# Optimization experiments

Hardware: AMD Instinct MI355X
Metric: run time of the kernel (lower is better)

Reference implementation:

```python
import jax, jax.numpy as jnp
import numpy as np

B, C_IN, HW = 4096, 3, 32
NUM_MODULES, NUM_AGENTS, OUT_DIM = 16, 10, 10
FEAT = 128
HID = 48
BN_EPS = 1e-5


def _conv_block(x, w, b):
    # x: [B,C,H,W], w: [O,I,3,3] -> conv(pad=1) + ReLU + maxpool2
    y = jax.lax.conv_general_dilated(
        x, w, window_strides=(1, 1), padding=((1, 1), (1, 1)),
        dimension_numbers=("NCHW", "OIHW", "NCHW"))
    y = jax.nn.relu(y + b[None, :, None, None])
    return jax.lax.reduce_window(y, -jnp.inf, jax.lax.max,
                                 (1, 1, 2, 2), (1, 1, 2, 2), "VALID")


def setup_inputs() -> dict:
    key = jax.random.key(0)
    ks = jax.random.split(key, 24)

    def lin(k, shape, fan_in):
        return (jax.random.normal(k, shape, dtype=jnp.float32) / np.sqrt(fan_in)).astype(jnp.float32)

    inp = {
        "x": jax.random.normal(ks[0], (B, C_IN, HW, HW), dtype=jnp.float32),
        "tasks": jax.random.randint(ks[1], (B,), 0, NUM_AGENTS, dtype=jnp.int32),
        # conv backbone
        "cw1": lin(ks[2], (32, C_IN, 3, 3), C_IN * 9), "cb1": jnp.zeros((32,), jnp.float32),
        "cw2": lin(ks[3], (32, 32, 3, 3), 32 * 9),     "cb2": jnp.zeros((32,), jnp.float32),
        "cw3": lin(ks[4], (32, 32, 3, 3), 32 * 9),     "cb3": jnp.zeros((32,), jnp.float32),
        "cw4": lin(ks[5], (32, 32, 3, 3), 32 * 9),     "cb4": jnp.zeros((32,), jnp.float32),
        "bn_g": jnp.ones((32,), jnp.float32), "bn_b": jnp.zeros((32,), jnp.float32),
        # routing policies (approx linear policies)
        "wpt": lin(ks[6], (FEAT, NUM_AGENTS), FEAT),                  # per-task assignment (1 agent)
        "wd1": lin(ks[7], (NUM_AGENTS, FEAT, NUM_MODULES), FEAT),    # per-agent decision 1
        "wd2": lin(ks[8], (NUM_AGENTS, HID, NUM_MODULES), HID),      # per-agent decision 2
        "wd3": lin(ks[9], (NUM_AGENTS, HID, NUM_MODULES), HID),      # per-agent decision 3
        # expert banks (stacked Linear layers, stored [in,out])
        "s1_w": lin(ks[10], (NUM_MODULES, FEAT, HID), FEAT), "s1_b": jnp.zeros((NUM_MODULES, HID), jnp.float32),
        "s2_w": lin(ks[11], (NUM_MODULES, HID, HID), HID),   "s2_b": jnp.zeros((NUM_MODULES, HID), jnp.float32),
        "s3_w": lin(ks[12], (NUM_MODULES, HID, OUT_DIM), HID), "s3_b": jnp.zeros((NUM_MODULES, OUT_DIM), jnp.float32),
    }
    return inp


def _decide(feat, wd, agents):
    # gather per-sample agent policy, pick argmax action
    logits = jnp.einsum("bf,bfm->bm", feat, wd[agents])  # [B, num_modules]
    return jnp.argmax(logits, axis=-1)


def _select(feat, w_bank, b_bank, actions, relu=True):
    # per-sample expert gather -> small GEMM -> scatter back (vectorized)
    y = jnp.einsum("bf,bfo->bo", feat, w_bank[actions]) + b_bank[actions]
    return jax.nn.relu(y) if relu else y


def reference(x, tasks, cw1, cb1, cw2, cb2, cw3, cb3, cw4, cb4, bn_g, bn_b,
              wpt, wd1, wd2, wd3, s1_w, s1_b, s2_w, s2_b, s3_w, s3_b):
    y = _conv_block(x, cw1, cb1)
    y = _conv_block(y, cw2, cb2)
    y = _conv_block(y, cw3, cb3)
    y = _conv_block(y, cw4, cb4)
    # BatchNorm2d (training-mode batch stats)
    mu = jnp.mean(y, axis=(0, 2, 3), keepdims=True)
    var = jnp.var(y, axis=(0, 2, 3), keepdims=True)
    y = (y - mu) * jax.lax.rsqrt(var + BN_EPS) * bn_g[None, :, None, None] + bn_b[None, :, None, None]
    y = y.reshape(y.shape[0], -1)  # [B, 128]

    # per-task assignment: single-agent policy picks the agent id per sample
    task_actions = jnp.argmax(y @ wpt, axis=-1)  # [B]

    a1 = _decide(y, wd1, task_actions)
    y = _select(y, s1_w, s1_b, a1, relu=True)
    a2 = _decide(y, wd2, task_actions)
    y = _select(y, s2_w, s2_b, a2, relu=True)
    a3 = _decide(y, wd3, task_actions)
    y = _select(y, s3_w, s3_b, a3, relu=False)
    return y
```

## Files before the change

kernel.cpp:

```cpp
#include <hip/hip_runtime.h>
#include <math.h>


#define IMG_B 4096

typedef _Float16 f16x8 __attribute__((ext_vector_type(8)));
typedef _Float16 f16x4 __attribute__((ext_vector_type(4)));
typedef float    f32x4 __attribute__((ext_vector_type(4)));

union U16x8 { unsigned u[4]; f16x8 v; };

__device__ inline f16x8 f16x8_zero() {
    f16x8 z;
    #pragma unroll
    for (int i = 0; i < 8; ++i) z[i] = (_Float16)0.f;
    return z;
}

__global__ __launch_bounds__(256) void twt_kernel(
    const float* __restrict__ cw1, const float* __restrict__ cw2,
    const float* __restrict__ cw3, const float* __restrict__ cw4,
    _Float16* __restrict__ w1s, _Float16* __restrict__ w2s,
    _Float16* __restrict__ w3s, _Float16* __restrict__ w4s)
{
    const int i = blockIdx.x * 256 + threadIdx.x;
    if (i < 2048) {
        const int p = i >> 10, rr = i & 1023;
        const int oc = rr >> 5, k = rr & 31;
        _Float16 val = (_Float16)0.f;
        if (k < 27) {
            float w = cw1[oc * 27 + k];
            _Float16 h = (_Float16)w;
            val = p ? (_Float16)(w - (float)h) : h;
        }
        w1s[p * 1024 + oc * 32 + k] = val;
    }
    if (i < 9216) {
        const int k = i % 9, r = i / 9;
        const int ic2 = r & 31, oc2 = r >> 5;
        {
            float w = cw2[(oc2 * 32 + ic2) * 9 + k];
            _Float16 h = (_Float16)w;
            w2s[(k * 2 + 0) * 1024 + oc2 * 32 + ic2] = h;
            w2s[(k * 2 + 1) * 1024 + oc2 * 32 + ic2] = (_Float16)(w - (float)h);
        }
        {
            float w = cw3[(oc2 * 32 + ic2) * 9 + k];
            _Float16 h = (_Float16)w;
            w3s[(k * 2 + 0) * 1024 + oc2 * 32 + ic2] = h;
            w3s[(k * 2 + 1) * 1024 + oc2 * 32 + ic2] = (_Float16)(w - (float)h);
        }
        {
            float w = cw4[(oc2 * 32 + ic2) * 9 + k];
            _Float16 h = (_Float16)w;
            w4s[(k * 2 + 0) * 1024 + oc2 * 32 + ic2] = h;
            w4s[(k * 2 + 1) * 1024 + oc2 * 32 + ic2] = (_Float16)(w - (float)h);
        }
    }
}

__global__ __launch_bounds__(512, 6) void backbone_kernel(
    const float* __restrict__ x,
    const _Float16* __restrict__ w1s, const float* __restrict__ cb1,
    const _Float16* __restrict__ w2s, const float* __restrict__ cb2,
    const _Float16* __restrict__ w3s, const float* __restrict__ cb3,
    const _Float16* __restrict__ w4s, const float* __restrict__ cb4,
    float* __restrict__ t4)
{
    __shared__ __align__(16) unsigned char smem[50736];
    _Float16* b1h = (_Float16*)smem;
    _Float16* b1l = (_Float16*)(smem + 18432);
    unsigned char* region2 = smem + 36864;
    unsigned* sxu = (unsigned*)region2;
    _Float16* b2h = (_Float16*)region2;
    _Float16* b2l = (_Float16*)(region2 + 4096);
    _Float16* b3h = (_Float16*)(region2 + 8192);
    _Float16* b3l = (_Float16*)(region2 + 10496);
    float*    scr = (float*)region2;

    const int t = threadIdx.x;
    const int b = blockIdx.x;
    const int lane = t & 63;
    const int w  = __builtin_amdgcn_readfirstlane(t >> 6);
    const int wr = w >> 1;
    const int mh = w & 1;
    const int xl = lane & 15;
    const int g  = lane >> 4;
    const int aoff = xl * 32 + g * 8;

    for (int i = t; i < 396; i += 512) {
        const int p = i / 132, r = i - p * 132;
        int row, col;
        if (r < 34)       { row = 0;       col = r; }
        else if (r < 68)  { row = 33;      col = r - 34; }
        else if (r < 100) { row = r - 67;  col = 0; }
        else              { row = r - 99;  col = 33; }
        sxu[p * 1156 + row * 34 + col] = 0;
    }
    for (int i = t; i < 1024; i += 512) {
        const int j = i & 15, cs = (i >> 4) & 1, r = (i >> 5) & 15, P = i >> 9;
        ((unsigned*)(smem + P * 18432))[(r * 18 + (cs ? 17 : 0)) * 16 + j] = 0;
    }
    {
        const float* xb = x + (size_t)b * 3072;
        for (int i = t; i < 3072; i += 512) {
            const int ic = i >> 10, r = i & 1023;
            const float v = xb[i];
            const _Float16 h = (_Float16)v;
            const _Float16 l = (_Float16)(v - (float)h);
            const unsigned hu = (unsigned)__builtin_bit_cast(unsigned short, h);
            const unsigned lu = (unsigned)__builtin_bit_cast(unsigned short, l);
            sxu[ic * 1156 + ((r >> 5) + 1) * 34 + (r & 31) + 1] =
                __builtin_amdgcn_perm(lu, hu, 0x05040100u);
        }
    }
    __syncthreads();

    {
        const f16x8 ah0 = *(const f16x8*)(w1s + xl * 32 + g * 8);
        const f16x8 ah1 = *(const f16x8*)(w1s + (16 + xl) * 32 + g * 8);
        const f16x8 al0 = *(const f16x8*)(w1s + 1024 + xl * 32 + g * 8);
        const f16x8 al1 = *(const f16x8*)(w1s + 1024 + (16 + xl) * 32 + g * 8);
        const f32x4 cbias0 = *(const f32x4*)(cb1 + g * 4);
        const f32x4 cbias1 = *(const f32x4*)(cb1 + 16 + g * 4);

        int off_j[8];
        #pragma unroll
        for (int j = 0; j < 8; ++j) {
            int k = g * 8 + j; if (k > 26) k = 26;
            const int ic = k / 9, t9 = k - ic * 9;
            const int dy = t9 / 3, dx = t9 - dy * 3;
            off_j[j] = ic * 1156 + dy * 34 + dx;
        }

        for (int q = 0; q < 2; ++q) {
            const int rp = w * 2 + q;
            const int y0 = 2 * rp;
            for (int xt = 0; xt < 2; ++xt) {
                const int xpix = xt * 16 + xl;
                f32x4 acc[2][2];
                #pragma unroll
                for (int yy = 0; yy < 2; ++yy)
                    #pragma unroll
                    for (int m = 0; m < 2; ++m)
                        #pragma unroll
                        for (int r = 0; r < 4; ++r) acc[yy][m][r] = 0.f;
                #pragma unroll
                for (int yy = 0; yy < 2; ++yy) {
                    const int base = (y0 + yy) * 34 + xpix;
                    unsigned e[8];
                    #pragma unroll
                    for (int j = 0; j < 8; ++j) e[j] = sxu[off_j[j] + base];
                    U16x8 Bh, Bl;
                    #pragma unroll
                    for (int p = 0; p < 4; ++p) {
                        const unsigned e0 = e[2 * p], e1 = e[2 * p + 1];
                        Bh.u[p] = __builtin_amdgcn_perm(e1, e0, 0x05040100u);
                        Bl.u[p] = __builtin_amdgcn_perm(e1, e0, 0x07060302u);
                    }
                    acc[yy][0] = __builtin_amdgcn_mfma_f32_16x16x32_f16(ah0, Bh.v, acc[yy][0], 0, 0, 0);
                    acc[yy][0] = __builtin_amdgcn_mfma_f32_16x16x32_f16(ah0, Bl.v, acc[yy][0], 0, 0, 0);
                    acc[yy][0] = __builtin_amdgcn_mfma_f32_16x16x32_f16(al0, Bh.v, acc[yy][0], 0, 0, 0);
                    acc[yy][1] = __builtin_amdgcn_mfma_f32_16x16x32_f16(ah1, Bh.v, acc[yy][1], 0, 0, 0);
                    acc[yy][1] = __builtin_amdgcn_mfma_f32_16x16x32_f16(ah1, Bl.v, acc[yy][1], 0, 0, 0);
                    acc[yy][1] = __builtin_amdgcn_mfma_f32_16x16x32_f16(al1, Bh.v, acc[yy][1], 0, 0, 0);
                }
                #pragma unroll
                for (int m = 0; m < 2; ++m) {
                    f32x4 vv;
                    #pragma unroll
                    for (int r = 0; r < 4; ++r) {
                        float v = fmaxf(acc[0][m][r], acc[1][m][r]);
                        v = fmaxf(v, __shfl_xor(v, 1));
                        vv[r] = fmaxf(v + (m ? cbias1[r] : cbias0[r]), 0.f);
                    }
                    if ((xl & 1) == 0) {
                        const int c = xt * 8 + (xl >> 1) + 1;
                        const int grp = m * 2 + (g >> 1);
                        const int so = (grp + (c >> 1)) & 3;
                        const int e = (rp * 18 + c) * 32 + so * 8 + (g & 1) * 4;
                        f16x4 h4, l4;
                        #pragma unroll
                        for (int r = 0; r < 4; ++r) {
                            const _Float16 h = (_Float16)vv[r];
                            h4[r] = h;
                            l4[r] = (_Float16)(vv[r] - (float)h);
                        }
                        *(f16x4*)(b1h + e) = h4;
                        *(f16x4*)(b1l + e) = l4;
                    }
                }
            }
        }
    }
    __syncthreads();

    {
        for (int i = t; i < 1152; i += 512) ((unsigned*)(region2 + 8192))[i] = 0;

        f32x4 acc[2][2];
        #pragma unroll
        for (int j = 0; j < 2; ++j)
            #pragma unroll
            for (int m = 0; m < 2; ++m)
                #pragma unroll
                for (int r = 0; r < 4; ++r) acc[j][m][r] = 0.f;

        #pragma unroll
        for (int dy = 0; dy < 3; ++dy) {
            #pragma unroll
            for (int dx = 0; dx < 3; ++dx) {
                const _Float16* wb = w2s + (dy * 3 + dx) * 2048;
                const f16x8 ah0 = *(const f16x8*)(wb + aoff);
                const f16x8 ah1 = *(const f16x8*)(wb + 512 + aoff);
                const f16x8 al0 = *(const f16x8*)(wb + 1024 + aoff);
                const f16x8 al1 = *(const f16x8*)(wb + 1536 + aoff);

                const int cxs = xl + dx;
                const int so = (g + (cxs >> 1)) & 3;
                #pragma unroll
                for (int j = 0; j < 2; ++j) {
                    const int sy = 2 * w + j + dy - 1;
                    if ((unsigned)sy < 16u) {
                        const int e = (sy * 18 + cxs) * 32 + so * 8;
                        const f16x8 bh = *(const f16x8*)(b1h + e);
                        const f16x8 bl = *(const f16x8*)(b1l + e);
                        acc[j][0] = __builtin_amdgcn_mfma_f32_16x16x32_f16(ah0, bh, acc[j][0], 0, 0, 0);
                        acc[j][0] = __builtin_amdgcn_mfma_f32_16x16x32_f16(ah0, bl, acc[j][0], 0, 0, 0);
                        acc[j][0] = __builtin_amdgcn_mfma_f32_16x16x32_f16(al0, bh, acc[j][0], 0, 0, 0);
                        acc[j][1] = __builtin_amdgcn_mfma_f32_16x16x32_f16(ah1, bh, acc[j][1], 0, 0, 0);
                        acc[j][1] = __builtin_amdgcn_mfma_f32_16x16x32_f16(ah1, bl, acc[j][1], 0, 0, 0);
                        acc[j][1] = __builtin_amdgcn_mfma_f32_16x16x32_f16(al1, bh, acc[j][1], 0, 0, 0);
                    }
                }
            }
        }

        const f32x4 bias0 = *(const f32x4*)(cb2 + g * 4);
        const f32x4 bias1 = *(const f32x4*)(cb2 + 16 + g * 4);
        #pragma unroll
        for (int m = 0; m < 2; ++m) {
            f32x4 vv;
            #pragma unroll
            for (int r = 0; r < 4; ++r) {
                float v = fmaxf(acc[0][m][r], acc[1][m][r]);
                v = fmaxf(v, __shfl_xor(v, 1));
                vv[r] = fmaxf(v + (m ? bias1[r] : bias0[r]), 0.f);
            }
            if ((lane & 1) == 0) {
                const int pp = w * 8 + (xl >> 1);
                const int slot = m * 2 + (g >> 1);
                const int so2 = (slot + (pp >> 1)) & 3;
                const int e = pp * 32 + so2 * 8 + (g & 1) * 4;
                f16x4 h4, l4;
                #pragma unroll
                for (int r = 0; r < 4; ++r) {
                    const _Float16 h = (_Float16)vv[r];
                    h4[r] = h;
                    l4[r] = (_Float16)(vv[r] - (float)h);
                }
                *(f16x4*)(b2h + e) = h4;
                *(f16x4*)(b2l + e) = l4;
            }
        }
    }
    __syncthreads();

    {
        const int p = wr * 16 + xl;
        const int py3 = p >> 3, px3 = p & 7;
        f32x4 acc;
        #pragma unroll
        for (int r = 0; r < 4; ++r) acc[r] = 0.f;

        #pragma unroll
        for (int dy = 0; dy < 3; ++dy) {
            #pragma unroll
            for (int dx = 0; dx < 3; ++dx) {
                const _Float16* wb = w3s + (dy * 3 + dx) * 2048 + mh * 512;
                const f16x8 ah = *(const f16x8*)(wb + aoff);
                const f16x8 al = *(const f16x8*)(wb + 1024 + aoff);

                const int syL = py3 + dy - 1, sxL = px3 + dx - 1;
                const bool ok = ((unsigned)syL < 8u) && ((unsigned)sxL < 8u);
                const int cy = syL < 0 ? 0 : (syL > 7 ? 7 : syL);
                const int cx = sxL < 0 ? 0 : (sxL > 7 ? 7 : sxL);
                const int cp = cy * 8 + cx;
                const int so = (g + (cp >> 1)) & 3;
                const int e = cp * 32 + so * 8;
                f16x8 bh = *(const f16x8*)(b2h + e);
                f16x8 bl = *(const f16x8*)(b2l + e);
                if (!ok) { bh = f16x8_zero(); bl = f16x8_zero(); }
                acc = __builtin_amdgcn_mfma_f32_16x16x32_f16(ah, bh, acc, 0, 0, 0);
                acc = __builtin_amdgcn_mfma_f32_16x16x32_f16(ah, bl, acc, 0, 0, 0);
                acc = __builtin_amdgcn_mfma_f32_16x16x32_f16(al, bh, acc, 0, 0, 0);
            }
        }

        const f32x4 bias = *(const f32x4*)(cb3 + mh * 16 + g * 4);
        f32x4 vv;
        #pragma unroll
        for (int r = 0; r < 4; ++r) {
            float v = acc[r];
            v = fmaxf(v, __shfl_xor(v, 1));
            v = fmaxf(v, __shfl_xor(v, 8));
            vv[r] = fmaxf(v + bias[r], 0.f);
        }
        if ((lane & 9) == 0) {
            const int yr = wr;
            const int xr = (xl & 7) >> 1;
            const int pp3 = (yr + 1) * 6 + (xr + 1);
            const int grp = mh * 2 + (g >> 1);
            const int so = (grp + (pp3 >> 1)) & 3;
            const int e = pp3 * 32 + so * 8 + (g & 1) * 4;
            f16x4 h4, l4;
            #pragma unroll
            for (int r = 0; r < 4; ++r) {
                const _Float16 h = (_Float16)vv[r];
                h4[r] = h;
                l4[r] = (_Float16)(vv[r] - (float)h);
            }
            *(f16x4*)(b3h + e) = h4;
            *(f16x4*)(b3l + e) = l4;
        }
    }
    __syncthreads();

    {
        f32x4 a4;
        #pragma unroll
        for (int r = 0; r < 4; ++r) a4[r] = 0.f;

        for (int t9 = wr; t9 < 9; t9 += 4) {
            const _Float16* wb = w4s + t9 * 2048 + mh * 512;
            const f16x8 ah = *(const f16x8*)(wb + aoff);
            const f16x8 al = *(const f16x8*)(wb + 1024 + aoff);
            const int dy = t9 / 3, dx = t9 - dy * 3;
            const int pp3 = ((xl >> 2) + dy) * 6 + (xl & 3) + dx;
            const int so = (g + (pp3 >> 1)) & 3;
            const int e = pp3 * 32 + so * 8;
            const f16x8 bh = *(const f16x8*)(b3h + e);
            const f16x8 bl = *(const f16x8*)(b3l + e);
            a4 = __builtin_amdgcn_mfma_f32_16x16x32_f16(ah, bh, a4, 0, 0, 0);
            a4 = __builtin_amdgcn_mfma_f32_16x16x32_f16(ah, bl, a4, 0, 0, 0);
            a4 = __builtin_amdgcn_mfma_f32_16x16x32_f16(al, bh, a4, 0, 0, 0);
        }
        *(f32x4*)(scr + (w * 64 + lane) * 4) = a4;
        __syncthreads();

        if (w < 2) {
            f32x4 r0;
            #pragma unroll
            for (int r = 0; r < 4; ++r) r0[r] = 0.f;
            #pragma unroll
            for (int k = 0; k < 4; ++k) {
                const f32x4 p0 = *(const f32x4*)(scr + ((k * 2 + w) * 64 + lane) * 4);
                #pragma unroll
                for (int r = 0; r < 4; ++r) r0[r] += p0[r];
            }
            const f32x4 bias = *(const f32x4*)(cb4 + w * 16 + g * 4);
            const int y = xl >> 2, xx = xl & 3;
            f32x4 vv;
            #pragma unroll
            for (int r = 0; r < 4; ++r) {
                float v = r0[r];
                v = fmaxf(v, __shfl_xor(v, 1));
                v = fmaxf(v, __shfl_xor(v, 4));
                vv[r] = fmaxf(v + bias[r], 0.f);
            }
            if ((xl & 5) == 0) {
                const int oc0 = w * 16 + g * 4;
                #pragma unroll
                for (int r = 0; r < 4; ++r)
                    t4[(size_t)b * 128 + (oc0 + r) * 4 + (y >> 1) * 2 + (xx >> 1)] = vv[r];
            }
        }
    }
}

__global__ __launch_bounds__(256) void bnstats_kernel(
    const float* __restrict__ t4, float* __restrict__ mus, float* __restrict__ rss)
{
    __shared__ double ssum[256];
    __shared__ double ssq[256];
    const int c = blockIdx.x, t = threadIdx.x;
    double s = 0.0, q = 0.0;
    for (int j = t; j < 16384; j += 256) {
        float v = t4[(size_t)(j >> 2) * 128 + c * 4 + (j & 3)];
        s += (double)v;
        q += (double)v * (double)v;
    }
    ssum[t] = s; ssq[t] = q;
    __syncthreads();
    for (int w = 128; w > 0; w >>= 1) {
        if (t < w) { ssum[t] += ssum[t + w]; ssq[t] += ssq[t + w]; }
        __syncthreads();
    }
    if (t == 0) {
        double mu = ssum[0] / 16384.0;
        double var = ssq[0] / 16384.0 - mu * mu;
        mus[c] = (float)mu;
        rss[c] = (float)(1.0 / sqrt(var + 1e-5));
    }
}

__device__ __forceinline__ int wave_argmax16(double v, int idx) {
    #pragma unroll
    for (int d = 8; d >= 1; d >>= 1) {
        const double ov = __shfl_xor(v, d);
        const int oi = __shfl_xor(idx, d);
        if (ov > v || (ov == v && oi < idx)) { v = ov; idx = oi; }
    }
    return __shfl(idx, 0);
}

__global__ __launch_bounds__(256) void routing_kernel(
    const float* __restrict__ t4, const float* __restrict__ mus,
    const float* __restrict__ rss,
    const float* __restrict__ bng, const float* __restrict__ bnb,
    const float* __restrict__ wpt, const float* __restrict__ wd1,
    const float* __restrict__ wd2, const float* __restrict__ wd3,
    const float* __restrict__ s1w, const float* __restrict__ s1b,
    const float* __restrict__ s2w, const float* __restrict__ s2b,
    const float* __restrict__ s3w, const float* __restrict__ s3b,
    float* __restrict__ out)
{
    __shared__ float fs[4][128];
    __shared__ float h1s[4][48];
    __shared__ float h2s[4][48];
    const int t = threadIdx.x & 63;
    const int w = threadIdx.x >> 6;
    const int b = blockIdx.x * 4 + w;
    float* fw  = fs[w];
    float* h1w = h1s[w];
    float* h2w = h2s[w];

    for (int i = t; i < 128; i += 64) {
        const int c = i >> 2;
        const float v = t4[(size_t)b * 128 + i];
        fw[i] = (v - mus[c]) * rss[c] * bng[c] + bnb[c];
    }
    __builtin_amdgcn_wave_barrier();

    double a = -INFINITY;
    if (t < 10) {
        a = 0.0;
        for (int k = 0; k < 128; ++k) a = fma((double)fw[k], (double)wpt[k * 10 + t], a);
    }
    const int agent = wave_argmax16(a, t & 15);

    a = -INFINITY;
    if (t < 16) {
        a = 0.0;
        const float* wd = wd1 + (size_t)agent * 2048 + t;
        for (int k = 0; k < 128; ++k) a = fma((double)fw[k], (double)wd[k * 16], a);
    }
    const int a1 = wave_argmax16(a, t & 15);

    if (t < 48) {
        float acc = s1b[a1 * 48 + t];
        const float* wd = s1w + (size_t)a1 * 6144 + t;
        for (int k = 0; k < 128; ++k) acc = fmaf(fw[k], wd[k * 48], acc);
        h1w[t] = fmaxf(acc, 0.f);
    }
    __builtin_amdgcn_wave_barrier();

    a = -INFINITY;
    if (t < 16) {
        a = 0.0;
        const float* wd = wd2 + (size_t)agent * 768 + t;
        for (int k = 0; k < 48; ++k) a = fma((double)h1w[k], (double)wd[k * 16], a);
    }
    const int a2 = wave_argmax16(a, t & 15);

    if (t < 48) {
        float acc = s2b[a2 * 48 + t];
        const float* wd = s2w + (size_t)a2 * 2304 + t;
        for (int k = 0; k < 48; ++k) acc = fmaf(h1w[k], wd[k * 48], acc);
        h2w[t] = fmaxf(acc, 0.f);
    }
    __builtin_amdgcn_wave_barrier();

    a = -INFINITY;
    if (t < 16) {
        a = 0.0;
        const float* wd = wd3 + (size_t)agent * 768 + t;
        for (int k = 0; k < 48; ++k) a = fma((double)h2w[k], (double)wd[k * 16], a);
    }
    const int a3 = wave_argmax16(a, t & 15);

    if (t < 10) {
        float acc = s3b[a3 * 10 + t];
        const float* wd = s3w + (size_t)a3 * 480 + t;
        for (int k = 0; k < 48; ++k) acc = fmaf(h2w[k], wd[k * 10], acc);
        out[(size_t)b * 10 + t] = acc;
    }
}

extern "C" void kernel_launch(void* const* d_in, const int* in_sizes, int n_in,
                              void* d_out, int out_size, void* d_ws, size_t ws_size,
                              hipStream_t stream)
{
    (void)in_sizes; (void)n_in; (void)out_size; (void)ws_size;

    const float* x   = (const float*)d_in[0];
    const float* cw1 = (const float*)d_in[2];
    const float* cb1 = (const float*)d_in[3];
    const float* cw2 = (const float*)d_in[4];
    const float* cb2 = (const float*)d_in[5];
    const float* cw3 = (const float*)d_in[6];
    const float* cb3 = (const float*)d_in[7];
    const float* cw4 = (const float*)d_in[8];
    const float* cb4 = (const float*)d_in[9];
    const float* bng = (const float*)d_in[10];
    const float* bnb = (const float*)d_in[11];
    const float* wpt = (const float*)d_in[12];
    const float* wd1 = (const float*)d_in[13];
    const float* wd2 = (const float*)d_in[14];
    const float* wd3 = (const float*)d_in[15];
    const float* s1w = (const float*)d_in[16];
    const float* s1b = (const float*)d_in[17];
    const float* s2w = (const float*)d_in[18];
    const float* s2b = (const float*)d_in[19];
    const float* s3w = (const float*)d_in[20];
    const float* s3b = (const float*)d_in[21];
    float* out = (float*)d_out;

    float* t4  = (float*)d_ws;
    float* mus = t4 + (size_t)IMG_B * 128;
    float* rss = mus + 32;
    _Float16* w1s = (_Float16*)(rss + 32);
    _Float16* w2s = w1s + 2048;
    _Float16* w3s = w2s + 18432;
    _Float16* w4s = w3s + 18432;

    hipLaunchKernelGGL(twt_kernel, dim3(36), dim3(256), 0, stream,
                       cw1, cw2, cw3, cw4, w1s, w2s, w3s, w4s);
    hipLaunchKernelGGL(backbone_kernel, dim3(IMG_B), dim3(512), 0, stream,
                       x, w1s, cb1, w2s, cb2, w3s, cb3, w4s, cb4, t4);
    hipLaunchKernelGGL(bnstats_kernel, dim3(32), dim3(256), 0, stream, t4, mus, rss);
    hipLaunchKernelGGL(routing_kernel, dim3(IMG_B / 4), dim3(256), 0, stream,
                       t4, mus, rss, bng, bnb, wpt, wd1, wd2, wd3,
                       s1w, s1b, s2w, s2b, s3w, s3b, out);
}
```

Before: 193.9 us.

## Split BN stats into two-stage reduction, unroll conv1 loops, multi-accumulate routing dots

```diff
diff --git a/kernel.cpp b/kernel.cpp
--- a/kernel.cpp
+++ b/kernel.cpp
@@ -133,9 +133,11 @@
             off_j[j] = ic * 1156 + dy * 34 + dx;
         }
 
+        #pragma unroll
         for (int q = 0; q < 2; ++q) {
             const int rp = w * 2 + q;
             const int y0 = 2 * rp;
+            #pragma unroll
             for (int xt = 0; xt < 2; ++xt) {
                 const int xpix = xt * 16 + xl;
                 f32x4 acc[2][2];
@@ -378,29 +380,46 @@
     }
 }
 
-__global__ __launch_bounds__(256) void bnstats_kernel(
-    const float* __restrict__ t4, float* __restrict__ mus, float* __restrict__ rss)
+__global__ __launch_bounds__(256) void bnstatsA_kernel(
+    const float* __restrict__ t4, double* __restrict__ part)
 {
     __shared__ double ssum[256];
     __shared__ double ssq[256];
-    const int c = blockIdx.x, t = threadIdx.x;
-    double s = 0.0, q = 0.0;
-    for (int j = t; j < 16384; j += 256) {
-        float v = t4[(size_t)(j >> 2) * 128 + c * 4 + (j & 3)];
-        s += (double)v;
+    const int c = blockIdx.x >> 3, s = blockIdx.x & 7, t = threadIdx.x;
+    const float* base = t4 + (size_t)s * 512 * 128 + c * 4;
+    double sm = 0.0, q = 0.0;
+    for (int j = t; j < 2048; j += 256) {
+        const float v = base[(size_t)(j >> 2) * 128 + (j & 3)];
+        sm += (double)v;
         q += (double)v * (double)v;
     }
-    ssum[t] = s; ssq[t] = q;
+    ssum[t] = sm; ssq[t] = q;
     __syncthreads();
     for (int w = 128; w > 0; w >>= 1) {
         if (t < w) { ssum[t] += ssum[t + w]; ssq[t] += ssq[t + w]; }
         __syncthreads();
     }
     if (t == 0) {
-        double mu = ssum[0] / 16384.0;
-        double var = ssq[0] / 16384.0 - mu * mu;
-        mus[c] = (float)mu;
-        rss[c] = (float)(1.0 / sqrt(var + 1e-5));
+        part[(c * 8 + s) * 2]     = ssum[0];
+        part[(c * 8 + s) * 2 + 1] = ssq[0];
+    }
+}
+
+__global__ __launch_bounds__(256) void bnstatsB_kernel(
+    const double* __restrict__ part, float* __restrict__ mus, float* __restrict__ rss)
+{
+    const int t = threadIdx.x;
+    double sm = part[t * 2], q = part[t * 2 + 1];
+    #pragma unroll
+    for (int d = 1; d < 8; d <<= 1) {
+        sm += __shfl_xor(sm, d);
+        q += __shfl_xor(q, d);
+    }
+    if ((t & 7) == 0) {
+        const double mu = sm / 16384.0;
+        const double var = q / 16384.0 - mu * mu;
+        mus[t >> 3] = (float)mu;
+        rss[t >> 3] = (float)(1.0 / sqrt(var + 1e-5));
     }
 }
 
@@ -444,56 +463,95 @@
 
     double a = -INFINITY;
     if (t < 10) {
-        a = 0.0;
-        for (int k = 0; k < 128; ++k) a = fma((double)fw[k], (double)wpt[k * 10 + t], a);
+        double s0 = 0, s1 = 0, s2 = 0, s3 = 0;
+        for (int k = 0; k < 128; k += 4) {
+            s0 = fma((double)fw[k],     (double)wpt[k * 10 + t],       s0);
+            s1 = fma((double)fw[k + 1], (double)wpt[(k + 1) * 10 + t], s1);
+            s2 = fma((double)fw[k + 2], (double)wpt[(k + 2) * 10 + t], s2);
+            s3 = fma((double)fw[k + 3], (double)wpt[(k + 3) * 10 + t], s3);
+        }
+        a = (s0 + s1) + (s2 + s3);
     }
     const int agent = wave_argmax16(a, t & 15);
 
     a = -INFINITY;
     if (t < 16) {
-        a = 0.0;
         const float* wd = wd1 + (size_t)agent * 2048 + t;
-        for (int k = 0; k < 128; ++k) a = fma((double)fw[k], (double)wd[k * 16], a);
+        double s0 = 0, s1 = 0, s2 = 0, s3 = 0;
+        for (int k = 0; k < 128; k += 4) {
+            s0 = fma((double)fw[k],     (double)wd[k * 16],       s0);
+            s1 = fma((double)fw[k + 1], (double)wd[(k + 1) * 16], s1);
+            s2 = fma((double)fw[k + 2], (double)wd[(k + 2) * 16], s2);
+            s3 = fma((double)fw[k + 3], (double)wd[(k + 3) * 16], s3);
+        }
+        a = (s0 + s1) + (s2 + s3);
     }
     const int a1 = wave_argmax16(a, t & 15);
 
     if (t < 48) {
-        float acc = s1b[a1 * 48 + t];
         const float* wd = s1w + (size_t)a1 * 6144 + t;
-        for (int k = 0; k < 128; ++k) acc = fmaf(fw[k], wd[k * 48], acc);
-        h1w[t] = fmaxf(acc, 0.f);
+        float c0 = s1b[a1 * 48 + t], c1 = 0.f, c2 = 0.f, c3 = 0.f;
+        for (int k = 0; k < 128; k += 4) {
+            c0 = fmaf(fw[k],     wd[k * 48],       c0);
+            c1 = fmaf(fw[k + 1], wd[(k + 1) * 48], c1);
+            c2 = fmaf(fw[k + 2], wd[(k + 2) * 48], c2);
+            c3 = fmaf(fw[k + 3], wd[(k + 3) * 48], c3);
+        }
+        h1w[t] = fmaxf((c0 + c1) + (c2 + c3), 0.f);
     }
     __builtin_amdgcn_wave_barrier();
 
     a = -INFINITY;
     if (t < 16) {
-        a = 0.0;
         const float* wd = wd2 + (size_t)agent * 768 + t;
-        for (int k = 0; k < 48; ++k) a = fma((double)h1w[k], (double)wd[k * 16], a);
+        double s0 = 0, s1 = 0, s2 = 0, s3 = 0;
+        for (int k = 0; k < 48; k += 4) {
+            s0 = fma((double)h1w[k],     (double)wd[k * 16],       s0);
+            s1 = fma((double)h1w[k + 1], (double)wd[(k + 1) * 16], s1);
+            s2 = fma((double)h1w[k + 2], (double)wd[(k + 2) * 16], s2);
+            s3 = fma((double)h1w[k + 3], (double)wd[(k + 3) * 16], s3);
+        }
+        a = (s0 + s1) + (s2 + s3);
     }
     const int a2 = wave_argmax16(a, t & 15);
 
     if (t < 48) {
-        float acc = s2b[a2 * 48 + t];
         const float* wd = s2w + (size_t)a2 * 2304 + t;
-        for (int k = 0; k < 48; ++k) acc = fmaf(h1w[k], wd[k * 48], acc);
-        h2w[t] = fmaxf(acc, 0.f);
+        float c0 = s2b[a2 * 48 + t], c1 = 0.f, c2 = 0.f, c3 = 0.f;
+        for (int k = 0; k < 48; k += 4) {
+            c0 = fmaf(h1w[k],     wd[k * 48],       c0);
+            c1 = fmaf(h1w[k + 1], wd[(k + 1) * 48], c1);
+            c2 = fmaf(h1w[k + 2], wd[(k + 2) * 48], c2);
+            c3 = fmaf(h1w[k + 3], wd[(k + 3) * 48], c3);
+        }
+        h2w[t] = fmaxf((c0 + c1) + (c2 + c3), 0.f);
     }
     __builtin_amdgcn_wave_barrier();
 
     a = -INFINITY;
     if (t < 16) {
-        a = 0.0;
         const float* wd = wd3 + (size_t)agent * 768 + t;
-        for (int k = 0; k < 48; ++k) a = fma((double)h2w[k], (double)wd[k * 16], a);
+        double s0 = 0, s1 = 0, s2 = 0, s3 = 0;
+        for (int k = 0; k < 48; k += 4) {
+            s0 = fma((double)h2w[k],     (double)wd[k * 16],       s0);
+            s1 = fma((double)h2w[k + 1], (double)wd[(k + 1) * 16], s1);
+            s2 = fma((double)h2w[k + 2], (double)wd[(k + 2) * 16], s2);
+            s3 = fma((double)h2w[k + 3], (double)wd[(k + 3) * 16], s3);
+        }
+        a = (s0 + s1) + (s2 + s3);
     }
     const int a3 = wave_argmax16(a, t & 15);
 
     if (t < 10) {
-        float acc = s3b[a3 * 10 + t];
         const float* wd = s3w + (size_t)a3 * 480 + t;
-        for (int k = 0; k < 48; ++k) acc = fmaf(h2w[k], wd[k * 10], acc);
-        out[(size_t)b * 10 + t] = acc;
+        float c0 = s3b[a3 * 10 + t], c1 = 0.f, c2 = 0.f, c3 = 0.f;
+        for (int k = 0; k < 48; k += 4) {
+            c0 = fmaf(h2w[k],     wd[k * 10],       c0);
+            c1 = fmaf(h2w[k + 1], wd[(k + 1) * 10], c1);
+            c2 = fmaf(h2w[k + 2], wd[(k + 2) * 10], c2);
+            c3 = fmaf(h2w[k + 3], wd[(k + 3) * 10], c3);
+        }
+        out[(size_t)b * 10 + t] = (c0 + c1) + (c2 + c3);
     }
 }
 
@@ -533,12 +591,14 @@
     _Float16* w2s = w1s + 2048;
     _Float16* w3s = w2s + 18432;
     _Float16* w4s = w3s + 18432;
+    double* part = (double*)(w4s + 18432);
 
     hipLaunchKernelGGL(twt_kernel, dim3(36), dim3(256), 0, stream,
                        cw1, cw2, cw3, cw4, w1s, w2s, w3s, w4s);
     hipLaunchKernelGGL(backbone_kernel, dim3(IMG_B), dim3(512), 0, stream,
                        x, w1s, cb1, w2s, cb2, w3s, cb3, w4s, cb4, t4);
-    hipLaunchKernelGGL(bnstats_kernel, dim3(32), dim3(256), 0, stream, t4, mus, rss);
+    hipLaunchKernelGGL(bnstatsA_kernel, dim3(256), dim3(256), 0, stream, t4, part);
+    hipLaunchKernelGGL(bnstatsB_kernel, dim3(1), dim3(256), 0, stream, part, mus, rss);
     hipLaunchKernelGGL(routing_kernel, dim3(IMG_B / 4), dim3(256), 0, stream,
                        t4, mus, rss, bng, bnb, wpt, wd1, wd2, wd3,
                        s1w, s1b, s2w, s2b, s3w, s3b, out);
```

After: 175.2 us (median of 2 runs). -9.6%, faster.
